# Performance work log

Measured on AMD Instinct MI355X. Metric: run time of the kernel, lower is better.

The kernel has to match this reference:

```python
import jax, jax.numpy as jnp
import numpy as np

H = 8            # num heads
K_ORDER = 3      # polynomial filter order


def setup_inputs() -> dict:
    key = jax.random.key(0)
    ks = jax.random.split(key, 7)
    B, N, D = 4, 2048, 256
    s = 0.05  # weight scale to keep softmax/poly numerically tame
    x = jax.random.normal(ks[0], (B, N, D), jnp.float32)
    Wq = jax.random.normal(ks[1], (D, D), jnp.float32) * s
    Wk = jax.random.normal(ks[2], (D, D), jnp.float32) * s
    Wv = jax.random.normal(ks[3], (D, D), jnp.float32) * s
    Wo = jax.random.normal(ks[4], (D, D), jnp.float32) * s
    coeffs = jax.random.normal(ks[5], (H, K_ORDER + 1), jnp.float32) * 0.5
    z = jnp.zeros((D,), jnp.float32)
    return {"x": x, "Wq": Wq, "bq": z, "Wk": Wk, "bk": z,
            "Wv": Wv, "bv": z, "Wo": Wo, "bo": z, "coeffs": coeffs}


def reference(x, Wq, bq, Wk, bk, Wv, bv, Wo, bo, coeffs):
    B, N, D = x.shape
    hd = D // H

    def split_heads(t):  # [B,N,D] -> [B,H,N,hd]
        return t.reshape(B, N, H, hd).transpose(0, 2, 1, 3)

    q = split_heads(x @ Wq + bq)
    k = split_heads(x @ Wk + bk)
    v = split_heads(x @ Wv + bv)

    # Estimator: learned adjacency via scaled-dot-product softmax, [B,H,N,N]
    scale = jnp.asarray(1.0 / np.sqrt(hd), x.dtype)
    A = jax.nn.softmax(jnp.einsum('bhnd,bhmd->bhnm', q, k) * scale, axis=-1)

    # Filter: X' = sum_{k=0}^{K} c[h,k] * A^k V
    out = coeffs[None, :, 0, None, None] * v
    t = v
    for kk in range(1, K_ORDER + 1):
        t = jnp.einsum('bhnm,bhmd->bhnd', A, t)
        out = out + coeffs[None, :, kk, None, None] * t

    merged = out.transpose(0, 2, 1, 3).reshape(B, N, D)  # concat heads
    return merged @ Wo + bo
```

## Files before the change

kernel.cpp:

```cpp
#include <hip/hip_runtime.h>
#include <hip/hip_bf16.h>

typedef __hip_bfloat16 bf16;
typedef __attribute__((ext_vector_type(8))) short short8;
typedef __attribute__((ext_vector_type(4))) float f32x4;

#define BB 4
#define NN 2048
#define DD 256
#define HH 8
#define HD 32
#define BN (BB*NN)
#define ELEMS (BN*DD)

__device__ int g_isf32;
__device__ __attribute__((aligned(256))) unsigned short g_qb [ELEMS];
__device__ __attribute__((aligned(256))) unsigned short g_kb [ELEMS];
__device__ __attribute__((aligned(256))) unsigned short g_tA [ELEMS];
__device__ __attribute__((aligned(256))) unsigned short g_tB [ELEMS];
__device__ __attribute__((aligned(256))) float          g_acc[ELEMS];
__device__ __attribute__((aligned(256))) unsigned short g_wt [4*DD*DD];
__device__ __attribute__((aligned(256))) float g_bias[4*DD];
__device__ __attribute__((aligned(256))) float g_cf[HH*4];

__device__ __forceinline__ float b2f(unsigned short u) {
    union { unsigned int i; float f; } c; c.i = ((unsigned int)u) << 16; return c.f;
}
__device__ __forceinline__ unsigned short f2b(float f) {
    bf16 h = __float2bfloat16(f);
    return *reinterpret_cast<unsigned short*>(&h);
}
__device__ __forceinline__ unsigned int pack2f(float a, float b) {
    unsigned int ua = __float_as_uint(a), ub = __float_as_uint(b);
    ua = (ua + 0x7FFFu + ((ua >> 16) & 1u)) >> 16;
    ub = (ub + 0x7FFFu + ((ub >> 16) & 1u)) & 0xFFFF0000u;
    return ua | ub;
}
__device__ __forceinline__ float ldin(const void* p, int i, int f32m) {
    return f32m ? ((const float*)p)[i] : b2f(((const unsigned short*)p)[i]);
}

__global__ __launch_bounds__(256) void probe_kernel(const void* __restrict__ x)
{
    __shared__ int cnt;
    if (threadIdx.x == 0) cnt = 0;
    __syncthreads();
    const unsigned short* u = (const unsigned short*)x;
    int w = 0;
    for (int i = threadIdx.x; i < 1024; i += 256) {
        const int e = (u[2 * i] >> 7) & 0xFF;
        if (e < 100 || e > 140) ++w;
    }
    atomicAdd(&cnt, w);
    __syncthreads();
    if (threadIdx.x == 0) g_isf32 = (cnt > 300) ? 1 : 0;
}

__global__ __launch_bounds__(256) void prep_w_kernel(
    const void* W0, const void* W1, const void* W2, const void* W3,
    const void* bq, const void* bk, const void* bv, const void* bo,
    const void* coeffs)
{
    const int f32m = g_isf32;
    __shared__ unsigned short tile[64][65];
    const int mat = blockIdx.y;
    const void* W = (mat == 0) ? W0 : (mat == 1) ? W1 : (mat == 2) ? W2 : W3;
    const int k0 = (blockIdx.x >> 2) * 64;
    const int n0 = (blockIdx.x & 3) * 64;
    const int t  = threadIdx.x;

    if (blockIdx.x == 0 && blockIdx.y == 0) {
        g_bias[0 * DD + t] = ldin(bq, t, f32m);
        g_bias[1 * DD + t] = ldin(bk, t, f32m);
        g_bias[2 * DD + t] = ldin(bv, t, f32m);
        g_bias[3 * DD + t] = ldin(bo, t, f32m);
        if (t < 32) g_cf[t] = ldin(coeffs, t, f32m);
    }

    #pragma unroll
    for (int it = 0; it < 16; ++it) {
        const int flat = it * 256 + t;
        const int i = flat >> 6, j = flat & 63;
        tile[j][i] = f2b(ldin(W, (k0 + i) * DD + n0 + j, f32m));
    }
    __syncthreads();
    unsigned short* wt = g_wt + mat * DD * DD;
    #pragma unroll
    for (int it = 0; it < 16; ++it) {
        const int flat = it * 256 + t;
        const int nl = flat >> 6, kl = flat & 63;
        wt[(n0 + nl) * DD + k0 + kl] = tile[nl][kl];
    }
}

__global__ __launch_bounds__(256) void qkv_gemm_kernel(const void* __restrict__ x)
{
    __shared__ unsigned short xs[64 * 32];
    __shared__ unsigned short wl[64 * 32];
    const int f32m = g_isf32;
    const int t  = threadIdx.x;
    const int w  = t >> 6, l = t & 63, lg = l >> 4, ln = l & 15;
    const int r0 = blockIdx.x * 64;
    const int n0 = blockIdx.y * 64;
    const int mat = blockIdx.z;
    const unsigned short* wt = g_wt + mat * DD * DD;
    const int sr = t >> 2, sc = (t & 3) * 8;

    f32x4 acc[4] = {{0,0,0,0},{0,0,0,0},{0,0,0,0},{0,0,0,0}};

    for (int kc = 0; kc < DD; kc += 32) {
        __syncthreads();
        if (f32m) {
            const float* src = (const float*)x + (size_t)(r0 + sr) * DD + kc + sc;
            const float4 a = *(const float4*)src;
            const float4 b = *(const float4*)(src + 4);
            union { uint4 v; unsigned short s[8]; } o;
            o.s[0]=f2b(a.x); o.s[1]=f2b(a.y); o.s[2]=f2b(a.z); o.s[3]=f2b(a.w);
            o.s[4]=f2b(b.x); o.s[5]=f2b(b.y); o.s[6]=f2b(b.z); o.s[7]=f2b(b.w);
            *(uint4*)(xs + sr * 32 + sc) = o.v;
        } else {
            *(uint4*)(xs + sr * 32 + sc) =
                *(const uint4*)((const unsigned short*)x + (size_t)(r0 + sr) * DD + kc + sc);
        }
        *(uint4*)(wl + sr * 32 + sc) =
            *(const uint4*)(wt + (size_t)(n0 + sr) * DD + kc + sc);
        __syncthreads();
        const short8 af = *(const short8*)(xs + (w * 16 + ln) * 32 + lg * 8);
        #pragma unroll
        for (int s = 0; s < 4; ++s) {
            const short8 bfr = *(const short8*)(wl + (s * 16 + ln) * 32 + lg * 8);
            acc[s] = __builtin_amdgcn_mfma_f32_16x16x32_bf16(af, bfr, acc[s], 0, 0, 0);
        }
    }

    const float QS = 0.17677669529663687f * 1.4426950408889634f;
    #pragma unroll
    for (int s = 0; s < 4; ++s) {
        const int j = n0 + s * 16 + ln;
        const float bias = g_bias[mat * DD + j];
        const int h = j >> 5, dd = j & 31;
        #pragma unroll
        for (int r = 0; r < 4; ++r) {
            const int rn = r0 + w * 16 + lg * 4 + r;
            const int b = rn >> 11, n = rn & (NN - 1);
            const int bh = b * HH + h;
            const float val = acc[s][r] + bias;
            if (mat == 0) {
                g_qb[((size_t)bh * NN + n) * HD + dd] = f2b(val * QS);
            } else if (mat == 1) {
                g_kb[((size_t)bh * NN + n) * HD + dd] = f2b(val);
            } else {
                g_tA[((size_t)bh * HD + dd) * NN + n] = f2b(val);
                g_acc[(size_t)rn * DD + j] = g_cf[h * 4] * val;
            }
        }
    }
}

__global__ __launch_bounds__(256) void attn_pass_kernel(const int kidx, const int dir)
{
    __shared__ float osh[4][32][33];
    __shared__ float lsh[4][32];

    const unsigned short* __restrict__ tin  = dir ? g_tB : g_tA;
    unsigned short*       __restrict__ tout = dir ? g_tA : g_tB;

    const int tid = threadIdx.x;
    const int w   = tid >> 6;
    const int l   = tid & 63;
    const int lg  = l >> 4;
    const int ln  = l & 15;

    const int bh = blockIdx.x >> 6;
    const int qt = blockIdx.x & 63;
    const int h  = bh & (HH - 1);
    const int b  = bh >> 3;
    const int q0 = qt * 32;

    short8 qf[2];
    #pragma unroll
    for (int qi = 0; qi < 2; ++qi)
        qf[qi] = *(const short8*)(g_qb +
            ((size_t)bh * NN + q0 + qi * 16 + ln) * HD + lg * 8);

    const unsigned short* kb = g_kb + (size_t)bh * NN * HD;
    const unsigned short* tb = tin  + (size_t)bh * HD * NN;

    f32x4 oacc[2][2] = {{{0,0,0,0},{0,0,0,0}},{{0,0,0,0},{0,0,0,0}}};
    float lsum[2] = {0.f, 0.f};
    const f32x4 zero = {0.f, 0.f, 0.f, 0.f};

    for (int it = 0; it < 16; ++it) {
        const int k0 = it * 128 + w * 32;
        const short8 kf0 = *(const short8*)(kb + (size_t)(k0 + ln) * HD + lg * 8);
        const short8 kf1 = *(const short8*)(kb + (size_t)(k0 + 16 + ln) * HD + lg * 8);
        const short8 tf0 = *(const short8*)(tb + (size_t)ln * NN + k0 + lg * 8);
        const short8 tf1 = *(const short8*)(tb + (size_t)(ln + 16) * NN + k0 + lg * 8);

        #pragma unroll
        for (int qi = 0; qi < 2; ++qi) {
            f32x4 s0 = __builtin_amdgcn_mfma_f32_16x16x32_bf16(kf0, qf[qi], zero, 0, 0, 0);
            f32x4 s1 = __builtin_amdgcn_mfma_f32_16x16x32_bf16(kf1, qf[qi], zero, 0, 0, 0);

            float p[8];
            #pragma unroll
            for (int r = 0; r < 4; ++r) {
                p[r]     = __builtin_amdgcn_exp2f(s0[r]);
                p[4 + r] = __builtin_amdgcn_exp2f(s1[r]);
                lsum[qi] += p[r] + p[4 + r];
            }
            const unsigned int pk0 = pack2f(p[0], p[1]);
            const unsigned int pk1 = pack2f(p[2], p[3]);
            const unsigned int pk2 = pack2f(p[4], p[5]);
            const unsigned int pk3 = pack2f(p[6], p[7]);

            int bi[4];
            #pragma unroll
            for (int j = 0; j < 4; ++j) {
                const int srcLane = (((2 * lg + (j >> 1)) & 3) << 4) + ln;
                const int lo = __shfl((j & 1) ? (int)pk1 : (int)pk0, srcLane, 64);
                const int hi = __shfl((j & 1) ? (int)pk3 : (int)pk2, srcLane, 64);
                bi[j] = (lg < 2) ? lo : hi;
            }
            union { int i[4]; short8 s; } pf;
            pf.i[0] = bi[0]; pf.i[1] = bi[1]; pf.i[2] = bi[2]; pf.i[3] = bi[3];

            oacc[qi][0] = __builtin_amdgcn_mfma_f32_16x16x32_bf16(tf0, pf.s, oacc[qi][0], 0, 0, 0);
            oacc[qi][1] = __builtin_amdgcn_mfma_f32_16x16x32_bf16(tf1, pf.s, oacc[qi][1], 0, 0, 0);
        }
    }

    #pragma unroll
    for (int qi = 0; qi < 2; ++qi) {
        lsum[qi] += __shfl_xor(lsum[qi], 16, 64);
        lsum[qi] += __shfl_xor(lsum[qi], 32, 64);
    }
    if (lg == 0) { lsh[w][ln] = lsum[0]; lsh[w][16 + ln] = lsum[1]; }

    #pragma unroll
    for (int qi = 0; qi < 2; ++qi)
        #pragma unroll
        for (int hf = 0; hf < 2; ++hf)
            #pragma unroll
            for (int r = 0; r < 4; ++r)
                osh[w][qi * 16 + ln][hf * 16 + lg * 4 + r] = oacc[qi][hf][r];
    __syncthreads();

    {
        const int q  = tid & 31;
        const int db = (tid >> 5) * 4;
        const float invl = 1.0f / (lsh[0][q] + lsh[1][q] + lsh[2][q] + lsh[3][q]);
        const float ck = g_cf[h * 4 + kidx];
        #pragma unroll
        for (int dd = 0; dd < 4; ++dd) {
            const int d = db + dd;
            const float val = (osh[0][q][d] + osh[1][q][d] +
                               osh[2][q][d] + osh[3][q][d]) * invl;
            tout[((size_t)bh * HD + d) * NN + q0 + q] = f2b(val);
            float* ga = g_acc + ((size_t)(b * NN + q0 + q)) * DD + h * HD + d;
            *ga += ck * val;
        }
    }
}

__global__ __launch_bounds__(256) void out_gemm_kernel(void* __restrict__ out)
{
    __shared__ unsigned short xs[64 * 32];
    __shared__ unsigned short wl[64 * 32];
    const int f32m = g_isf32;
    const int t  = threadIdx.x;
    const int w  = t >> 6, l = t & 63, lg = l >> 4, ln = l & 15;
    const int r0 = blockIdx.x * 64;
    const int n0 = blockIdx.y * 64;
    const unsigned short* wt = g_wt + 3 * DD * DD;
    const int sr = t >> 2, sc = (t & 3) * 8;

    f32x4 acc[4] = {{0,0,0,0},{0,0,0,0},{0,0,0,0},{0,0,0,0}};

    for (int kc = 0; kc < DD; kc += 32) {
        __syncthreads();
        {
            const float* src = g_acc + (size_t)(r0 + sr) * DD + kc + sc;
            const float4 a = *(const float4*)src;
            const float4 b = *(const float4*)(src + 4);
            union { uint4 v; unsigned short s[8]; } o;
            o.s[0]=f2b(a.x); o.s[1]=f2b(a.y); o.s[2]=f2b(a.z); o.s[3]=f2b(a.w);
            o.s[4]=f2b(b.x); o.s[5]=f2b(b.y); o.s[6]=f2b(b.z); o.s[7]=f2b(b.w);
            *(uint4*)(xs + sr * 32 + sc) = o.v;
        }
        *(uint4*)(wl + sr * 32 + sc) =
            *(const uint4*)(wt + (size_t)(n0 + sr) * DD + kc + sc);
        __syncthreads();
        const short8 af = *(const short8*)(xs + (w * 16 + ln) * 32 + lg * 8);
        #pragma unroll
        for (int s = 0; s < 4; ++s) {
            const short8 bfr = *(const short8*)(wl + (s * 16 + ln) * 32 + lg * 8);
            acc[s] = __builtin_amdgcn_mfma_f32_16x16x32_bf16(af, bfr, acc[s], 0, 0, 0);
        }
    }

    #pragma unroll
    for (int s = 0; s < 4; ++s) {
        const int j = n0 + s * 16 + ln;
        const float bias = g_bias[3 * DD + j];
        #pragma unroll
        for (int r = 0; r < 4; ++r) {
            const int rn = r0 + w * 16 + lg * 4 + r;
            const float val = acc[s][r] + bias;
            if (f32m) ((float*)out)[(size_t)rn * DD + j] = val;
            else      ((bf16*)out)[(size_t)rn * DD + j] = __float2bfloat16(val);
        }
    }
}

extern "C" void kernel_launch(void* const* d_in, const int* in_sizes, int n_in,
                              void* d_out, int out_size, void* d_ws, size_t ws_size,
                              hipStream_t stream)
{
    const void* x      = d_in[0];
    const void* Wq     = d_in[1];
    const void* bq     = d_in[2];
    const void* Wk     = d_in[3];
    const void* bk     = d_in[4];
    const void* Wv     = d_in[5];
    const void* bv     = d_in[6];
    const void* Wo     = d_in[7];
    const void* bo     = d_in[8];
    const void* coeffs = d_in[9];
    (void)d_ws; (void)ws_size; (void)in_sizes; (void)n_in; (void)out_size;

    probe_kernel<<<1, 256, 0, stream>>>(x);

    prep_w_kernel<<<dim3(16, 4), 256, 0, stream>>>(Wq, Wk, Wv, Wo,
                                                   bq, bk, bv, bo, coeffs);

    qkv_gemm_kernel<<<dim3(128, 4, 3), 256, 0, stream>>>(x);

    const int agrid = (BB * HH) * (NN / 32);
    attn_pass_kernel<<<agrid, 256, 0, stream>>>(1, 0);
    attn_pass_kernel<<<agrid, 256, 0, stream>>>(2, 1);
    attn_pass_kernel<<<agrid, 256, 0, stream>>>(3, 0);

    out_gemm_kernel<<<dim3(128, 4), 256, 0, stream>>>(d_out);
}
```

Measured before the change: 260.1 us.

## Widen attention query tile to 64 and drop P shuffles via 16x16x16 MFMA

Each attention block now handles 64 queries instead of 32, so every K and T fragment load feeds twice as many MFMAs and the grid is halved. The P-times-T product now uses the 16x16x16 bf16 MFMA, whose input layout matches the score output layout, so the cross-lane shuffles that repacked P are removed. The software bf16 rounding is replaced by the hardware packed convert when it is available. In exchange, register pressure and shared memory per block grow, and with fewer blocks occupancy may drop.

```diff
diff --git a/kernel.cpp b/kernel.cpp
--- a/kernel.cpp
+++ b/kernel.cpp
@@ -3,6 +3,7 @@
 
 typedef __hip_bfloat16 bf16;
 typedef __attribute__((ext_vector_type(8))) short short8;
+typedef __attribute__((ext_vector_type(4))) short short4v;
 typedef __attribute__((ext_vector_type(4))) float f32x4;
 
 #define BB 4
@@ -30,12 +31,21 @@
     bf16 h = __float2bfloat16(f);
     return *reinterpret_cast<unsigned short*>(&h);
 }
-__device__ __forceinline__ unsigned int pack2f(float a, float b) {
+#if __has_builtin(__builtin_amdgcn_cvt_pk_bf16_f32)
+typedef __attribute__((ext_vector_type(2))) __bf16 bf16x2t;
+__device__ __forceinline__ unsigned int pk2(float a, float b) {
+    union { bf16x2t v; unsigned int u; } c;
+    c.v = __builtin_amdgcn_cvt_pk_bf16_f32(a, b);
+    return c.u;
+}
+#else
+__device__ __forceinline__ unsigned int pk2(float a, float b) {
     unsigned int ua = __float_as_uint(a), ub = __float_as_uint(b);
     ua = (ua + 0x7FFFu + ((ua >> 16) & 1u)) >> 16;
     ub = (ub + 0x7FFFu + ((ub >> 16) & 1u)) & 0xFFFF0000u;
     return ua | ub;
 }
+#endif
 __device__ __forceinline__ float ldin(const void* p, int i, int f32m) {
     return f32m ? ((const float*)p)[i] : b2f(((const unsigned short*)p)[i]);
 }
@@ -159,8 +169,8 @@
 
 __global__ __launch_bounds__(256) void attn_pass_kernel(const int kidx, const int dir)
 {
-    __shared__ float osh[4][32][33];
-    __shared__ float lsh[4][32];
+    __shared__ float osh[4][64][33];
+    __shared__ float lsh[4][64];
 
     const unsigned short* __restrict__ tin  = dir ? g_tB : g_tA;
     unsigned short*       __restrict__ tout = dir ? g_tA : g_tB;
@@ -171,37 +181,45 @@
     const int lg  = l >> 4;
     const int ln  = l & 15;
 
-    const int bh = blockIdx.x >> 6;
-    const int qt = blockIdx.x & 63;
+    const int bh = blockIdx.x >> 5;
+    const int qt = blockIdx.x & 31;
     const int h  = bh & (HH - 1);
     const int b  = bh >> 3;
-    const int q0 = qt * 32;
-
-    short8 qf[2];
-    #pragma unroll
-    for (int qi = 0; qi < 2; ++qi)
+    const int q0 = qt * 64;
+
+    short8 qf[4];
+    #pragma unroll
+    for (int qi = 0; qi < 4; ++qi)
         qf[qi] = *(const short8*)(g_qb +
             ((size_t)bh * NN + q0 + qi * 16 + ln) * HD + lg * 8);
 
     const unsigned short* kb = g_kb + (size_t)bh * NN * HD;
     const unsigned short* tb = tin  + (size_t)bh * HD * NN;
 
-    f32x4 oacc[2][2] = {{{0,0,0,0},{0,0,0,0}},{{0,0,0,0},{0,0,0,0}}};
-    float lsum[2] = {0.f, 0.f};
+    f32x4 oacc[4][2];
+    #pragma unroll
+    for (int qi = 0; qi < 4; ++qi) { oacc[qi][0] = (f32x4){0,0,0,0}; oacc[qi][1] = (f32x4){0,0,0,0}; }
+    float lsum[4] = {0.f, 0.f, 0.f, 0.f};
     const f32x4 zero = {0.f, 0.f, 0.f, 0.f};
 
     for (int it = 0; it < 16; ++it) {
         const int k0 = it * 128 + w * 32;
         const short8 kf0 = *(const short8*)(kb + (size_t)(k0 + ln) * HD + lg * 8);
         const short8 kf1 = *(const short8*)(kb + (size_t)(k0 + 16 + ln) * HD + lg * 8);
-        const short8 tf0 = *(const short8*)(tb + (size_t)ln * NN + k0 + lg * 8);
-        const short8 tf1 = *(const short8*)(tb + (size_t)(ln + 16) * NN + k0 + lg * 8);
-
-        #pragma unroll
-        for (int qi = 0; qi < 2; ++qi) {
+
+#if __has_builtin(__builtin_amdgcn_mfma_f32_16x16x16bf16_1k)
+        short4v tf[2][2];
+        #pragma unroll
+        for (int c = 0; c < 2; ++c)
+            #pragma unroll
+            for (int hf = 0; hf < 2; ++hf)
+                tf[c][hf] = *(const short4v*)(tb +
+                    (size_t)(hf * 16 + ln) * NN + k0 + c * 16 + lg * 4);
+
+        #pragma unroll
+        for (int qi = 0; qi < 4; ++qi) {
             f32x4 s0 = __builtin_amdgcn_mfma_f32_16x16x32_bf16(kf0, qf[qi], zero, 0, 0, 0);
             f32x4 s1 = __builtin_amdgcn_mfma_f32_16x16x32_bf16(kf1, qf[qi], zero, 0, 0, 0);
-
             float p[8];
             #pragma unroll
             for (int r = 0; r < 4; ++r) {
@@ -209,36 +227,60 @@
                 p[4 + r] = __builtin_amdgcn_exp2f(s1[r]);
                 lsum[qi] += p[r] + p[4 + r];
             }
-            const unsigned int pk0 = pack2f(p[0], p[1]);
-            const unsigned int pk1 = pack2f(p[2], p[3]);
-            const unsigned int pk2 = pack2f(p[4], p[5]);
-            const unsigned int pk3 = pack2f(p[6], p[7]);
-
+            union { unsigned int u[2]; short4v s; } pb0, pb1;
+            pb0.u[0] = pk2(p[0], p[1]); pb0.u[1] = pk2(p[2], p[3]);
+            pb1.u[0] = pk2(p[4], p[5]); pb1.u[1] = pk2(p[6], p[7]);
+            oacc[qi][0] = __builtin_amdgcn_mfma_f32_16x16x16bf16_1k(tf[0][0], pb0.s, oacc[qi][0], 0, 0, 0);
+            oacc[qi][1] = __builtin_amdgcn_mfma_f32_16x16x16bf16_1k(tf[0][1], pb0.s, oacc[qi][1], 0, 0, 0);
+            oacc[qi][0] = __builtin_amdgcn_mfma_f32_16x16x16bf16_1k(tf[1][0], pb1.s, oacc[qi][0], 0, 0, 0);
+            oacc[qi][1] = __builtin_amdgcn_mfma_f32_16x16x16bf16_1k(tf[1][1], pb1.s, oacc[qi][1], 0, 0, 0);
+        }
+#else
+        const short8 tf0 = *(const short8*)(tb + (size_t)ln * NN + k0 + lg * 8);
+        const short8 tf1 = *(const short8*)(tb + (size_t)(ln + 16) * NN + k0 + lg * 8);
+        #pragma unroll
+        for (int qi = 0; qi < 4; ++qi) {
+            f32x4 s0 = __builtin_amdgcn_mfma_f32_16x16x32_bf16(kf0, qf[qi], zero, 0, 0, 0);
+            f32x4 s1 = __builtin_amdgcn_mfma_f32_16x16x32_bf16(kf1, qf[qi], zero, 0, 0, 0);
+            float p[8];
+            #pragma unroll
+            for (int r = 0; r < 4; ++r) {
+                p[r]     = __builtin_amdgcn_exp2f(s0[r]);
+                p[4 + r] = __builtin_amdgcn_exp2f(s1[r]);
+                lsum[qi] += p[r] + p[4 + r];
+            }
+            const unsigned int pk0 = pk2(p[0], p[1]);
+            const unsigned int pk1 = pk2(p[2], p[3]);
+            const unsigned int pk2v = pk2(p[4], p[5]);
+            const unsigned int pk3 = pk2(p[6], p[7]);
             int bi[4];
             #pragma unroll
             for (int j = 0; j < 4; ++j) {
                 const int srcLane = (((2 * lg + (j >> 1)) & 3) << 4) + ln;
                 const int lo = __shfl((j & 1) ? (int)pk1 : (int)pk0, srcLane, 64);
-                const int hi = __shfl((j & 1) ? (int)pk3 : (int)pk2, srcLane, 64);
+                const int hi = __shfl((j & 1) ? (int)pk3 : (int)pk2v, srcLane, 64);
                 bi[j] = (lg < 2) ? lo : hi;
             }
             union { int i[4]; short8 s; } pf;
             pf.i[0] = bi[0]; pf.i[1] = bi[1]; pf.i[2] = bi[2]; pf.i[3] = bi[3];
-
             oacc[qi][0] = __builtin_amdgcn_mfma_f32_16x16x32_bf16(tf0, pf.s, oacc[qi][0], 0, 0, 0);
             oacc[qi][1] = __builtin_amdgcn_mfma_f32_16x16x32_bf16(tf1, pf.s, oacc[qi][1], 0, 0, 0);
         }
-    }
-
-    #pragma unroll
-    for (int qi = 0; qi < 2; ++qi) {
+#endif
+    }
+
+    #pragma unroll
+    for (int qi = 0; qi < 4; ++qi) {
         lsum[qi] += __shfl_xor(lsum[qi], 16, 64);
         lsum[qi] += __shfl_xor(lsum[qi], 32, 64);
     }
-    if (lg == 0) { lsh[w][ln] = lsum[0]; lsh[w][16 + ln] = lsum[1]; }
-
-    #pragma unroll
-    for (int qi = 0; qi < 2; ++qi)
+    if (lg == 0) {
+        #pragma unroll
+        for (int qi = 0; qi < 4; ++qi) lsh[w][qi * 16 + ln] = lsum[qi];
+    }
+
+    #pragma unroll
+    for (int qi = 0; qi < 4; ++qi)
         #pragma unroll
         for (int hf = 0; hf < 2; ++hf)
             #pragma unroll
@@ -247,12 +289,12 @@
     __syncthreads();
 
     {
-        const int q  = tid & 31;
-        const int db = (tid >> 5) * 4;
+        const int q  = tid & 63;
+        const int db = (tid >> 6) * 8;
         const float invl = 1.0f / (lsh[0][q] + lsh[1][q] + lsh[2][q] + lsh[3][q]);
         const float ck = g_cf[h * 4 + kidx];
         #pragma unroll
-        for (int dd = 0; dd < 4; ++dd) {
+        for (int dd = 0; dd < 8; ++dd) {
             const int d = db + dd;
             const float val = (osh[0][q][d] + osh[1][q][d] +
                                osh[2][q][d] + osh[3][q][d]) * invl;
@@ -336,7 +378,7 @@
 
     qkv_gemm_kernel<<<dim3(128, 4, 3), 256, 0, stream>>>(x);
 
-    const int agrid = (BB * HH) * (NN / 32);
+    const int agrid = (BB * HH) * (NN / 64);
     attn_pass_kernel<<<agrid, 256, 0, stream>>>(1, 0);
     attn_pass_kernel<<<agrid, 256, 0, stream>>>(2, 1);
     attn_pass_kernel<<<agrid, 256, 0, stream>>>(3, 0);
```

Result: faster. 240.4 us (-7.6%).
